# Optimization experiments

Hardware: AMD Instinct MI355X
Metric: run time of the kernel (lower is better)

The kernel has to match this reference:

```python
import jax, jax.numpy as jnp
import numpy as np

B, L, D, H = 8, 4096, 1024, 16
HD = D // H
HID = 4096  # int(D * 4.0)
KSZ = 25    # moving-average kernel size
EPS = 1e-6


def _layernorm(x, w, b):
    mu = jnp.mean(x, axis=-1, keepdims=True)
    var = jnp.mean((x - mu) ** 2, axis=-1, keepdims=True)
    return (x - mu) / jnp.sqrt(var + EPS) * w + b


def _lin(x, W, b):
    # eqx.nn.Linear stores weight as (out, in)
    return jnp.einsum('...i,oi->...o', x, W) + b


def setup_inputs() -> dict:
    key = jax.random.key(0)
    ks = jax.random.split(key, 8)
    s = 0.02
    return {
        'x': jax.random.normal(ks[0], (B, L, D), dtype=jnp.float32),
        'ln1_w': jnp.ones((D,), jnp.float32),
        'ln1_b': jnp.zeros((D,), jnp.float32),
        'Wq': jax.random.normal(ks[1], (D, D), jnp.float32) * s,
        'bq': jnp.zeros((D,), jnp.float32),
        'Wk': jax.random.normal(ks[2], (D, D), jnp.float32) * s,
        'bk': jnp.zeros((D,), jnp.float32),
        'Wv': jax.random.normal(ks[3], (D, D), jnp.float32) * s,
        'bv': jnp.zeros((D,), jnp.float32),
        'Wo': jax.random.normal(ks[4], (D, D), jnp.float32) * s,
        'bo': jnp.zeros((D,), jnp.float32),
        'ln2_w': jnp.ones((D,), jnp.float32),
        'ln2_b': jnp.zeros((D,), jnp.float32),
        'W1': jax.random.normal(ks[5], (HID, D), jnp.float32) * s,
        'b1': jnp.zeros((HID,), jnp.float32),
        'W2': jax.random.normal(ks[6], (D, HID), jnp.float32) * s,
        'b2': jnp.zeros((D,), jnp.float32),
    }


def reference(x, ln1_w, ln1_b, Wq, bq, Wk, bk, Wv, bv, Wo, bo,
              ln2_w, ln2_b, W1, b1, W2, b2):
    b, l, d = x.shape
    # --- AutoCorrelation attention on norm1(x) ---
    y = _layernorm(x, ln1_w, ln1_b)
    Q = _lin(y, Wq, bq).reshape(b, l, H, HD).transpose(0, 2, 1, 3)  # (B,H,L,hd)
    K = _lin(y, Wk, bk).reshape(b, l, H, HD).transpose(0, 2, 1, 3)
    V = _lin(y, Wv, bv).reshape(b, l, H, HD).transpose(0, 2, 1, 3)
    qf = jnp.fft.rfft(Q, axis=2)
    kf = jnp.fft.rfft(K, axis=2)
    corr_time = jnp.fft.irfft(qf * jnp.conjugate(kf), n=l, axis=2)  # (B,H,L,hd)
    corr = jnp.mean(corr_time, axis=-1)                             # (B,H,L)
    attn = jax.nn.softmax(corr, axis=-1)
    out = jnp.einsum('bhl,bhld->bhd', attn, V)                      # (B,H,hd)
    # faithful lossy reshape: transpose(0,2,1) -> (B,hd,H), flatten to (B,D)
    out = out.transpose(0, 2, 1).reshape(b, d)
    out = _lin(out, Wo, bo)
    y = jnp.broadcast_to(out[:, None, :], (b, l, d))  # repeat over L
    x = x + y
    # --- Series decomposition: depthwise moving average, subtract trend ---
    kern = jnp.ones((KSZ, 1, d), x.dtype) / KSZ
    xt = x.transpose(0, 2, 1)  # (B,D,L)
    trend = jax.lax.conv_general_dilated(
        xt, kern, window_strides=(1,), padding='SAME',
        dimension_numbers=('NCL', 'LIO', 'NCL'), feature_group_count=d)
    x = x - trend.transpose(0, 2, 1)
    # --- MLP (dropout p=0 -> identity) ---
    y = _layernorm(x, ln2_w, ln2_b)
    y = _lin(jax.nn.gelu(_lin(y, W1, b1)), W2, b2)
    return x + y
```

## Files before the change

### kernel.cpp

```cpp
#include <hip/hip_runtime.h>

#define DEV __device__ __forceinline__

typedef __attribute__((ext_vector_type(8))) short bf16x8;
typedef __attribute__((ext_vector_type(4))) float f32x4;
typedef unsigned short u16;
typedef __attribute__((address_space(1))) const void* gvp;
typedef __attribute__((address_space(3))) void* svp;

DEV u16 f2bf(float f){
  unsigned u = __float_as_uint(f);
  u = (u + 0x7FFFu + ((u >> 16) & 1u)) >> 16;
  return (u16)u;
}
DEV float bf2f(u16 v){ return __uint_as_float(((unsigned)v) << 16); }
DEV float2 cmul(float2 a, float2 b){ return make_float2(a.x*b.x - a.y*b.y, a.x*b.y + a.y*b.x); }
DEV int rev8(int i){
  return ((i & 7) << 9) | ((i & 0x38) << 3) | ((i & 0x1C0) >> 3) | ((i >> 9) & 7);
}

__global__ void k_prep(const float* __restrict__ Wq, const float* __restrict__ Wk,
                       const float* __restrict__ W1, const float* __restrict__ W2,
                       const float* __restrict__ bq, const float* __restrict__ bk,
                       u16* __restrict__ Wqkb, u16* __restrict__ W1b, u16* __restrict__ W2b,
                       float* __restrict__ bqk, float2* __restrict__ twg){
  const size_t i = (size_t)blockIdx.x * 256 + threadIdx.x;
  if (i < 1048576){
    Wqkb[i] = f2bf(Wq[i]);
  } else if (i < 2097152){
    Wqkb[i] = f2bf(Wk[i - 1048576]);
  } else if (i < 6291456){
    W1b[i - 2097152] = f2bf(W1[i - 2097152]);
  } else if (i < 10485760){
    W2b[i - 6291456] = f2bf(W2[i - 6291456]);
  } else if (i < 10487808){
    const int k = (int)(i - 10485760);
    float sn, cs;
    sincosf(-1.5339807878856412e-03f * (float)k, &sn, &cs);
    twg[k] = make_float2(cs, sn);
  } else if (i < 10488832){
    const int k = (int)(i - 10487808);
    bqk[k] = bq[k]; bqk[1024 + k] = bk[k];
  }
}

__global__ __launch_bounds__(256) void k_ln(const float* __restrict__ x, const float* __restrict__ w,
                                            const float* __restrict__ b, u16* __restrict__ y){
  const int row = blockIdx.x;
  const int tid = threadIdx.x;
  const float4 v = ((const float4*)(x + (size_t)row * 1024))[tid];
  float s1 = v.x + v.y + v.z + v.w;
  float s2 = v.x*v.x + v.y*v.y + v.z*v.z + v.w*v.w;
  #pragma unroll
  for (int o = 32; o > 0; o >>= 1){ s1 += __shfl_down(s1, o); s2 += __shfl_down(s2, o); }
  __shared__ float r1[4], r2[4];
  __shared__ float mu_s, rs_s;
  const int wv = tid >> 6;
  if ((tid & 63) == 0){ r1[wv] = s1; r2[wv] = s2; }
  __syncthreads();
  if (tid == 0){
    float t1 = r1[0]+r1[1]+r1[2]+r1[3], t2 = r2[0]+r2[1]+r2[2]+r2[3];
    float mu = t1 * (1.0f/1024.0f);
    float var = t2 * (1.0f/1024.0f) - mu*mu;
    mu_s = mu; rs_s = rsqrtf(var + 1e-6f);
  }
  __syncthreads();
  const float mu = mu_s, rs = rs_s;
  const float4 wv4 = ((const float4*)w)[tid];
  const float4 bv4 = ((const float4*)b)[tid];
  ushort4 o4;
  o4.x = f2bf((v.x-mu)*rs*wv4.x + bv4.x);
  o4.y = f2bf((v.y-mu)*rs*wv4.y + bv4.y);
  o4.z = f2bf((v.z-mu)*rs*wv4.z + bv4.z);
  o4.w = f2bf((v.w-mu)*rs*wv4.w + bv4.w);
  ((ushort4*)(y + (size_t)row*1024))[tid] = o4;
}

template<int MODE>
__launch_bounds__(512, 2)
__global__ void k_gemm5(const u16* __restrict__ A, const u16* __restrict__ Bw,
                        const float* __restrict__ bias, void* __restrict__ out, void* __restrict__ out2,
                        int M, int N, int K)
{
  __shared__ __align__(16) u16 SMEM[65536];
  u16 (*LA)[16384] = reinterpret_cast<u16(*)[16384]>(SMEM);
  u16 (*LB)[16384] = reinterpret_cast<u16(*)[16384]>(SMEM + 32768);
  const int tid = threadIdx.x;
  const int wave = tid >> 6, lane = tid & 63;
  const int l15 = lane & 15, l4 = lane >> 4;
  const int wrq = wave >> 2, wcq = wave & 3;
  (void)M;

  const int nwg = gridDim.x;
  const int q8 = nwg >> 3;
  const int wg = (blockIdx.x & 7) * q8 + (blockIdx.x >> 3);
  const int NBN = N >> 8;
  const int bm = wg / NBN, bn = wg % NBN;
  const int NT = K >> 6, NI = NT >> 1;

  const int sr8 = lane >> 3;
  const int sch8 = ((lane & 7) ^ (sr8 & 7)) * 8;
  const u16* gA = A  + ((size_t)(bm*256 + wave*16 + sr8)) * K + sch8;
  const u16* gB = Bw + ((size_t)(bn*256 + wave*16 + sr8)) * K + sch8;
  const size_t gH = (size_t)128 * K;
  const size_t gJ = (size_t)8 * K;
  const int lbase = wave * 1024;

  const unsigned swzb = (unsigned)((l4 ^ (l15 & 7)) * 16);
  const unsigned uA0  = (unsigned)(uintptr_t)&LA[0][0] + (unsigned)((wrq*64 + l15)*128) + swzb;
  const unsigned uB0  = (unsigned)(uintptr_t)&LB[0][0] + (unsigned)((wcq*32 + l15)*128) + swzb;
  const unsigned uA0x = uA0 ^ 64u, uB0x = uB0 ^ 64u;
  const unsigned uA1  = uA0 + 32768u, uA1x = uA0x + 32768u;
  const unsigned uB1  = uB0 + 32768u, uB1x = uB0x + 32768u;

  f32x4 acc[8][4];
  const f32x4 z4 = {0.f, 0.f, 0.f, 0.f};
  #pragma unroll
  for (int m = 0; m < 8; ++m)
    #pragma unroll
    for (int n = 0; n < 4; ++n) acc[m][n] = z4;

#define DSR(dst, base, OFF) asm volatile("ds_read_b128 %0, %1 offset:" #OFF : "=v"(dst) : "v"(base))

#define LDA_Q0(b0, b1) do{ \
  DSR(fa[0], b0, 0);    DSR(fa[1], b1, 0); \
  DSR(fa[2], b0, 2048); DSR(fa[3], b1, 2048); \
  DSR(fa[4], b0, 4096); DSR(fa[5], b1, 4096); \
  DSR(fa[6], b0, 6144); DSR(fa[7], b1, 6144); }while(0)
#define LDA_Q1(b0, b1) do{ \
  DSR(fa[0], b0, 16384); DSR(fa[1], b1, 16384); \
  DSR(fa[2], b0, 18432); DSR(fa[3], b1, 18432); \
  DSR(fa[4], b0, 20480); DSR(fa[5], b1, 20480); \
  DSR(fa[6], b0, 22528); DSR(fa[7], b1, 22528); }while(0)
#define LDB_Q0(dst, b0, b1) do{ \
  DSR(dst[0], b0, 0);    DSR(dst[1], b1, 0); \
  DSR(dst[2], b0, 2048); DSR(dst[3], b1, 2048); }while(0)
#define LDB_Q1(dst, b0, b1) do{ \
  DSR(dst[0], b0, 16384); DSR(dst[1], b1, 16384); \
  DSR(dst[2], b0, 18432); DSR(dst[3], b1, 18432); }while(0)

#define STG(LD, G, DB, HALF, TK) do{ \
    const int tk_ = (TK) < NT ? (TK) : NT - 1; \
    const u16* g_ = (G) + (size_t)tk_ * 64 + (size_t)(HALF) * gH; \
    u16* l_ = &LD[DB][lbase + (HALF) * 8192]; \
    __builtin_amdgcn_global_load_lds((gvp)g_,        (svp)l_,        16, 0, 0); \
    __builtin_amdgcn_global_load_lds((gvp)(g_ + gJ), (svp)(l_ + 512),16, 0, 0); \
  }while(0)

#define MFMA16(QA, QB, FB) do{ \
    __builtin_amdgcn_s_setprio(1); \
    _Pragma("unroll") for (int kk = 0; kk < 2; ++kk) \
    _Pragma("unroll") for (int mm = 0; mm < 4; ++mm) \
    _Pragma("unroll") for (int nn = 0; nn < 2; ++nn) \
      acc[(QA)*4+mm][(QB)*2+nn] = __builtin_amdgcn_mfma_f32_16x16x32_bf16( \
          fa[mm*2+kk], FB[nn*2+kk], acc[(QA)*4+mm][(QB)*2+nn], 0, 0, 0); \
    __builtin_amdgcn_s_setprio(0); \
  }while(0)

#define SBAR  __builtin_amdgcn_s_barrier()
#define SB0   __builtin_amdgcn_sched_barrier(0)
#define LGKM0 do{ asm volatile("s_waitcnt lgkmcnt(0)" ::: "memory"); SB0; }while(0)
#define LGKM8 asm volatile("s_waitcnt lgkmcnt(8)" ::: "memory")
#define VM4   asm volatile("s_waitcnt vmcnt(4)" ::: "memory")

  STG(LA, gA, 0, 0, 0); STG(LA, gA, 0, 1, 0);
  STG(LB, gB, 0, 0, 0); STG(LB, gB, 0, 1, 0);
  STG(LA, gA, 1, 0, 1);
  STG(LB, gB, 1, 1, 1);
  VM4; SBAR;

  for (int it = 0; it < NI; ++it){
    const int u = 2 * it;
    bf16x8 fa[8], fbA[4], fbB[4];
    LDB_Q0(fbA, uB0, uB0x);
    LDA_Q0(uA0, uA0x);
    STG(LA, gA, 1, 1, u+1); STG(LB, gB, 1, 0, u+1);
    LGKM8;
    SBAR; LGKM0; MFMA16(0, 0, fbA); SB0; SBAR;
    LDB_Q1(fbB, uB0, uB0x);
    SBAR; LGKM0; MFMA16(0, 1, fbB); SB0; SBAR;
    LDA_Q1(uA0, uA0x);
    STG(LA, gA, 0, 0, u+2);
    SBAR; LGKM0; MFMA16(1, 1, fbB); SB0; SBAR;
    STG(LB, gB, 0, 1, u+2);
    VM4; SBAR; SB0; MFMA16(1, 0, fbA); SB0; SBAR;
    LDB_Q0(fbA, uB1, uB1x);
    LDA_Q0(uA1, uA1x);
    STG(LA, gA, 0, 1, u+2); STG(LB, gB, 0, 0, u+2);
    LGKM8;
    SBAR; LGKM0; MFMA16(0, 0, fbA); SB0; SBAR;
    LDB_Q1(fbB, uB1, uB1x);
    SBAR; LGKM0; MFMA16(0, 1, fbB); SB0; SBAR;
    LDA_Q1(uA1, uA1x);
    STG(LA, gA, 1, 0, u+3);
    SBAR; LGKM0; MFMA16(1, 1, fbB); SB0; SBAR;
    STG(LB, gB, 1, 1, u+3);
    VM4; SBAR; SB0; MFMA16(1, 0, fbA); SB0; SBAR;
  }
#undef DSR
#undef LDA_Q0
#undef LDA_Q1
#undef LDB_Q0
#undef LDB_Q1
#undef STG
#undef MFMA16
#undef SBAR
#undef SB0
#undef LGKM0
#undef LGKM8
#undef VM4

  if (MODE == 3){
    asm volatile("s_waitcnt vmcnt(0)" ::: "memory");
    __syncthreads();
    u16* T = SMEM;
    const int bq = bm >> 4;
    const int l0 = (bm & 15) * 256;
    u16* dstb = (u16*)(bn < 4 ? out : out2) + ((size_t)bq*1024 + (bn & 3)*256)*4096 + l0;
    #pragma unroll
    for (int half = 0; half < 2; ++half){
      #pragma unroll
      for (int nn = 0; nn < 2; ++nn){
        const int n = half*2 + nn;
        const int colh = wcq*32 + nn*16 + l15;
        const float bv = bias[bn*256 + half*128 + colh];
        #pragma unroll
        for (int m = 0; m < 8; ++m){
          const int lrow = (m>>2)*128 + wrq*64 + (m&3)*16 + l4*4;
          ushort4 o4;
          o4.x = f2bf(acc[m][n][0] + bv);
          o4.y = f2bf(acc[m][n][1] + bv);
          o4.z = f2bf(acc[m][n][2] + bv);
          o4.w = f2bf(acc[m][n][3] + bv);
          *(ushort4*)&T[colh*264 + lrow] = o4;
        }
      }
      __syncthreads();
      {
        const int c = tid >> 2, lch = (tid & 3) * 64;
        u16* drow = dstb + (size_t)(half*128 + c) * 4096 + lch;
        const u16* srow = &T[c*264 + lch];
        #pragma unroll
        for (int i = 0; i < 8; ++i)
          *(bf16x8*)(drow + i*8) = *(const bf16x8*)(srow + i*8);
      }
      __syncthreads();
    }
  } else {
    #pragma unroll
    for (int m = 0; m < 8; ++m){
      const int gr0 = bm*256 + (m>>2)*128 + wrq*64 + (m&3)*16 + l4*4;
      #pragma unroll
      for (int n = 0; n < 4; ++n){
        const int gc = bn*256 + (n>>1)*128 + wcq*32 + (n&1)*16 + l15;
        const float bv = bias[gc];
        #pragma unroll
        for (int r2 = 0; r2 < 4; ++r2){
          const size_t off = (size_t)(gr0 + r2) * N + gc;
          float v = acc[m][n][r2] + bv;
          if (MODE == 1){
            const float a = 0.7978845608028654f * (v + 0.044715f * v * v * v);
            const float e = __expf(2.0f * a);
            const float th = (e - 1.0f) / (e + 1.0f);
            ((u16*)out)[off] = f2bf(0.5f * v * (1.0f + th));
          } else {
            float* op = (float*)out;
            op[off] += v;
          }
        }
      }
    }
  }
}

DEV void fft4096_dif8(float2* Z, const float2* tw, int tid){
  const float C = 0.70710678118654752f;
  #pragma unroll
  for (int s = 4; s >= 1; --s){
    const int q = 1 << (3*(s-1));
    const int step = 1 << (12 - 3*s);
    #pragma unroll
    for (int tt = tid; tt < 512; tt += 256){
      const int j = tt & (q-1);
      const int base = ((tt >> (3*(s-1))) << (3*s)) + j;
      float2 a0 = Z[base],       a1 = Z[base+q],   a2 = Z[base+2*q], a3 = Z[base+3*q];
      float2 a4 = Z[base+4*q],   a5 = Z[base+5*q], a6 = Z[base+6*q], a7 = Z[base+7*q];
      float2 e0 = {a0.x+a4.x, a0.y+a4.y}, o0 = {a0.x-a4.x, a0.y-a4.y};
      float2 e1 = {a2.x+a6.x, a2.y+a6.y}, o1 = {a2.x-a6.x, a2.y-a6.y};
      float2 e2 = {a1.x+a5.x, a1.y+a5.y}, o2 = {a1.x-a5.x, a1.y-a5.y};
      float2 e3 = {a3.x+a7.x, a3.y+a7.y}, o3 = {a3.x-a7.x, a3.y-a7.y};
      float2 E0 = {e0.x+e1.x, e0.y+e1.y}, E1 = {e0.x-e1.x, e0.y-e1.y};
      float2 E2 = {e2.x+e3.x, e2.y+e3.y}, E3 = {e2.x-e3.x, e2.y-e3.y};
      float2 u0 = {E0.x+E2.x, E0.y+E2.y};
      float2 u4 = {E0.x-E2.x, E0.y-E2.y};
      float2 njE3 = {E3.y, -E3.x};
      float2 u2 = {E1.x+njE3.x, E1.y+njE3.y};
      float2 u6 = {E1.x-njE3.x, E1.y-njE3.y};
      float2 W1o2 = {C*(o2.x+o2.y), C*(o2.y-o2.x)};
      float2 W3o2 = {C*(o2.y-o2.x), -C*(o2.x+o2.y)};
      float2 W1o3 = {C*(o3.x+o3.y), C*(o3.y-o3.x)};
      float2 W3o3 = {C*(o3.y-o3.x), -C*(o3.x+o3.y)};
      float2 njo1 = {o1.y, -o1.x};
      float2 u1 = {o0.x + W1o2.x + njo1.x + W3o3.x, o0.y + W1o2.y + njo1.y + W3o3.y};
      float2 u3 = {o0.x + W3o2.x - njo1.x + W1o3.x, o0.y + W3o2.y - njo1.y + W1o3.y};
      float2 u5 = {o0.x - W1o2.x + njo1.x - W3o3.x, o0.y - W1o2.y + njo1.y - W3o3.y};
      float2 u7 = {o0.x - W3o2.x - njo1.x - W1o3.x, o0.y - W3o2.y - njo1.y - W1o3.y};
      const float2 w1 = tw[j*step];
      const float2 w2 = tw[2*j*step];
      const float2 w4 = tw[4*j*step];
      const float2 w3 = cmul(w1, w2);
      const float2 w5 = cmul(w1, w4);
      const float2 w6 = cmul(w2, w4);
      const float2 w7 = cmul(w3, w4);
      Z[base]     = u0;
      Z[base+q]   = cmul(u1, w1);
      Z[base+2*q] = cmul(u2, w2);
      Z[base+3*q] = cmul(u3, w3);
      Z[base+4*q] = cmul(u4, w4);
      Z[base+5*q] = cmul(u5, w5);
      Z[base+6*q] = cmul(u6, w6);
      Z[base+7*q] = cmul(u7, w7);
    }
    __syncthreads();
  }
}

DEV void fft4096_dit8_inv(float2* Z, const float2* tw, int tid){
  const float C = 0.70710678118654752f;
  #pragma unroll
  for (int s = 1; s <= 4; ++s){
    const int q = 1 << (3*(s-1));
    const int step = 1 << (12 - 3*s);
    #pragma unroll
    for (int tt = tid; tt < 512; tt += 256){
      const int j = tt & (q-1);
      const int base = ((tt >> (3*(s-1))) << (3*s)) + j;
      float2 a0 = Z[base],       a1 = Z[base+q],   a2 = Z[base+2*q], a3 = Z[base+3*q];
      float2 a4 = Z[base+4*q],   a5 = Z[base+5*q], a6 = Z[base+6*q], a7 = Z[base+7*q];
      float2 w1 = tw[j*step];   w1.y = -w1.y;
      float2 w2 = tw[2*j*step]; w2.y = -w2.y;
      float2 w4 = tw[4*j*step]; w4.y = -w4.y;
      const float2 w3 = cmul(w1, w2);
      const float2 w5 = cmul(w1, w4);
      const float2 w6 = cmul(w2, w4);
      const float2 w7 = cmul(w3, w4);
      a1 = cmul(a1, w1); a2 = cmul(a2, w2); a3 = cmul(a3, w3);
      a4 = cmul(a4, w4); a5 = cmul(a5, w5); a6 = cmul(a6, w6); a7 = cmul(a7, w7);
      float2 e0 = {a0.x+a4.x, a0.y+a4.y}, o0 = {a0.x-a4.x, a0.y-a4.y};
      float2 e1 = {a2.x+a6.x, a2.y+a6.y}, o1 = {a2.x-a6.x, a2.y-a6.y};
      float2 e2 = {a1.x+a5.x, a1.y+a5.y}, o2 = {a1.x-a5.x, a1.y-a5.y};
      float2 e3 = {a3.x+a7.x, a3.y+a7.y}, o3 = {a3.x-a7.x, a3.y-a7.y};
      float2 E0 = {e0.x+e1.x, e0.y+e1.y}, E1 = {e0.x-e1.x, e0.y-e1.y};
      float2 E2 = {e2.x+e3.x, e2.y+e3.y}, E3 = {e2.x-e3.x, e2.y-e3.y};
      float2 pjE3 = {-E3.y, E3.x};
      float2 W1o2 = {C*(o2.x-o2.y), C*(o2.x+o2.y)};
      float2 W3o2 = {-C*(o2.x+o2.y), C*(o2.x-o2.y)};
      float2 W1o3 = {C*(o3.x-o3.y), C*(o3.x+o3.y)};
      float2 W3o3 = {-C*(o3.x+o3.y), C*(o3.x-o3.y)};
      float2 pjo1 = {-o1.y, o1.x};
      Z[base]     = make_float2(E0.x+E2.x, E0.y+E2.y);
      Z[base+q]   = make_float2(o0.x + W1o2.x + pjo1.x + W3o3.x, o0.y + W1o2.y + pjo1.y + W3o3.y);
      Z[base+2*q] = make_float2(E1.x+pjE3.x, E1.y+pjE3.y);
      Z[base+3*q] = make_float2(o0.x + W3o2.x - pjo1.x + W1o3.x, o0.y + W3o2.y - pjo1.y + W1o3.y);
      Z[base+4*q] = make_float2(E0.x-E2.x, E0.y-E2.y);
      Z[base+5*q] = make_float2(o0.x - W1o2.x + pjo1.x - W3o3.x, o0.y - W1o2.y + pjo1.y - W3o3.y);
      Z[base+6*q] = make_float2(E1.x-pjE3.x, E1.y-pjE3.y);
      Z[base+7*q] = make_float2(o0.x - W3o2.x - pjo1.x - W1o3.x, o0.y - W3o2.y - pjo1.y - W1o3.y);
    }
    __syncthreads();
  }
}

__global__ __launch_bounds__(256) void k_fftcorr(const u16* __restrict__ Qt, const u16* __restrict__ Kt,
                                                 const float2* __restrict__ twg, float* __restrict__ S){
  __shared__ float2 Z[4096];
  __shared__ float2 tw[2048];
  const int tid = threadIdx.x;
  const int bh = blockIdx.x, dg = blockIdx.y;
  for (int k = tid; k < 2048; k += 256) tw[k] = twg[k];
  float2 sa[16];
  #pragma unroll
  for (int j = 0; j < 16; ++j) sa[j] = make_float2(0.f, 0.f);
  __syncthreads();
  for (int dd = 0; dd < 8; ++dd){
    const int d = dg*8 + dd;
    const u16* q  = Qt + ((size_t)bh*64 + d) * 4096;
    const u16* kp = Kt + ((size_t)bh*64 + d) * 4096;
    for (int i = tid; i < 4096; i += 256)
      Z[i] = make_float2(bf2f(q[i]), bf2f(kp[i]));
    __syncthreads();
    fft4096_dif8(Z, tw, tid);
    #pragma unroll
    for (int j = 0; j < 16; ++j){
      const int p = j*256 + tid;
      const int f = rev8(p);
      const int p2 = rev8((4096 - f) & 4095);
      const float2 a = Z[p];
      const float2 c = Z[p2];
      const float qr = 0.5f * (a.x + c.x);
      const float qi = 0.5f * (a.y - c.y);
      const float kr = 0.5f * (a.y + c.y);
      const float ki = 0.5f * (c.x - a.x);
      sa[j].x += qr*kr + qi*ki;
      sa[j].y += qi*kr - qr*ki;
    }
    __syncthreads();
  }
  float2* Sg = (float2*)S + ((size_t)dg*128 + bh) * 4096;
  #pragma unroll
  for (int j = 0; j < 16; ++j)
    Sg[j*256 + tid] = sa[j];
}

__global__ __launch_bounds__(256) void k_isoftmax(const float* __restrict__ S, const float2* __restrict__ twg,
                                                  float* __restrict__ attn){
  __shared__ float2 Z[4096];
  __shared__ float2 tw[2048];
  __shared__ float red[4];
  __shared__ float bc;
  const int tid = threadIdx.x;
  const int bh = blockIdx.x;
  for (int k = tid; k < 2048; k += 256) tw[k] = twg[k];
  const float2* S2 = (const float2*)S;
  for (int i = tid; i < 4096; i += 256){
    float2 acc = make_float2(0.f, 0.f);
    #pragma unroll
    for (int g = 0; g < 8; ++g){
      const float2 v = S2[((size_t)g*128 + bh) * 4096 + i];
      acc.x += v.x; acc.y += v.y;
    }
    Z[i] = acc;
  }
  __syncthreads();
  fft4096_dit8_inv(Z, tw, tid);
  const float scale = 1.0f / (4096.0f * 64.0f);
  float cr[16];
  float lmax = -1e30f;
  #pragma unroll
  for (int j = 0; j < 16; ++j){
    const float c = Z[j*256 + tid].x * scale;
    cr[j] = c;
    lmax = fmaxf(lmax, c);
  }
  #pragma unroll
  for (int o = 32; o > 0; o >>= 1) lmax = fmaxf(lmax, __shfl_down(lmax, o));
  if ((tid & 63) == 0) red[tid >> 6] = lmax;
  __syncthreads();
  if (tid == 0) bc = fmaxf(fmaxf(red[0], red[1]), fmaxf(red[2], red[3]));
  __syncthreads();
  const float gmax = bc;
  float lsum = 0.f;
  #pragma unroll
  for (int j = 0; j < 16; ++j){ cr[j] = __expf(cr[j] - gmax); lsum += cr[j]; }
  #pragma unroll
  for (int o = 32; o > 0; o >>= 1) lsum += __shfl_down(lsum, o);
  if ((tid & 63) == 0) red[tid >> 6] = lsum;
  __syncthreads();
  if (tid == 0) bc = red[0] + red[1] + red[2] + red[3];
  __syncthreads();
  const float inv = 1.0f / bc;
  float* at = attn + (size_t)bh * 4096;
  #pragma unroll
  for (int j = 0; j < 16; ++j) at[j*256 + tid] = cr[j] * inv;
}

__global__ __launch_bounds__(256) void k_yw(const float* __restrict__ attn, const u16* __restrict__ Y,
                                            float* __restrict__ yw){
  __shared__ float at[128*20 + 4];
  const int b = blockIdx.x, lq = blockIdx.y;
  const int l0 = lq * 128;
  const int tid = threadIdx.x;
  for (int idx = tid; idx < 2048; idx += 256){
    const int h = idx >> 7, l = idx & 127;
    at[l*20 + h] = attn[((size_t)b*16 + h)*4096 + l0 + l];
  }
  __syncthreads();
  float acc[16][4];
  #pragma unroll
  for (int h = 0; h < 16; ++h)
    #pragma unroll
    for (int j = 0; j < 4; ++j) acc[h][j] = 0.f;
  const u16* yb = Y + ((size_t)b*4096 + l0)*1024 + tid*4;
  for (int l = 0; l < 128; ++l){
    const ushort4 yv4 = *(const ushort4*)(yb + (size_t)l*1024);
    const float y0 = bf2f(yv4.x), y1 = bf2f(yv4.y), y2 = bf2f(yv4.z), y3 = bf2f(yv4.w);
    #pragma unroll
    for (int hq = 0; hq < 4; ++hq){
      const float4 a4 = *(const float4*)&at[l*20 + hq*4];
      acc[hq*4+0][0] += a4.x*y0; acc[hq*4+0][1] += a4.x*y1; acc[hq*4+0][2] += a4.x*y2; acc[hq*4+0][3] += a4.x*y3;
      acc[hq*4+1][0] += a4.y*y0; acc[hq*4+1][1] += a4.y*y1; acc[hq*4+1][2] += a4.y*y2; acc[hq*4+1][3] += a4.y*y3;
      acc[hq*4+2][0] += a4.z*y0; acc[hq*4+2][1] += a4.z*y1; acc[hq*4+2][2] += a4.z*y2; acc[hq*4+2][3] += a4.z*y3;
      acc[hq*4+3][0] += a4.w*y0; acc[hq*4+3][1] += a4.w*y1; acc[hq*4+3][2] += a4.w*y2; acc[hq*4+3][3] += a4.w*y3;
    }
  }
  float* ywb = yw + (size_t)b*16*1024 + tid*4;
  #pragma unroll
  for (int h = 0; h < 16; ++h)
    #pragma unroll
    for (int j = 0; j < 4; ++j)
      atomicAdd(&ywb[(size_t)h*1024 + j], acc[h][j]);
}

__global__ __launch_bounds__(256) void k_vproj(const float* __restrict__ yw, const float* __restrict__ Wv,
                                               const float* __restrict__ bv, float* __restrict__ oav){
  __shared__ float yv[1024];
  const int b = blockIdx.x, h = blockIdx.y;
  const int tid = threadIdx.x;
  for (int i = tid; i < 1024; i += 256) yv[i] = yw[((size_t)b*16 + h)*1024 + i];
  __syncthreads();
  const int hd = tid >> 2, q = tid & 3;
  const float4* wr = (const float4*)(Wv + (size_t)(h*64 + hd)*1024 + q*256);
  float acc = 0.f;
  #pragma unroll 4
  for (int i = 0; i < 64; ++i){
    const float4 w4 = wr[i];
    acc += yv[q*256+4*i]*w4.x + yv[q*256+4*i+1]*w4.y + yv[q*256+4*i+2]*w4.z + yv[q*256+4*i+3]*w4.w;
  }
  acc += __shfl_xor(acc, 1);
  acc += __shfl_xor(acc, 2);
  if (q == 0) oav[(size_t)b*1024 + hd*16 + h] = acc + bv[h*64 + hd];
}

__global__ __launch_bounds__(256) void k_proj(const float* __restrict__ oav, const float* __restrict__ Wo,
                                              const float* __restrict__ bo, float* __restrict__ proj){
  const int b = blockIdx.x;
  const int o = blockIdx.y * 256 + threadIdx.x;
  __shared__ float xin[1024];
  for (int i = threadIdx.x; i < 1024; i += 256) xin[i] = oav[(size_t)b*1024 + i];
  __syncthreads();
  float acc = bo[o];
  const float4* wr = (const float4*)(Wo + (size_t)o * 1024);
  #pragma unroll 4
  for (int i = 0; i < 256; ++i){
    const float4 w4 = wr[i];
    acc += xin[4*i]*w4.x + xin[4*i+1]*w4.y + xin[4*i+2]*w4.z + xin[4*i+3]*w4.w;
  }
  proj[(size_t)b*1024 + o] = acc;
}

__global__ __launch_bounds__(256) void k_decomp(const float* __restrict__ x, const float* __restrict__ proj,
                                                float* __restrict__ out){
  const int b = blockIdx.x, dq = blockIdx.y, lc = blockIdx.z;
  const int d = dq*256 + threadIdx.x;
  const int l0 = lc * 128;
  const float pv = proj[(size_t)b*1024 + d];
  const float* xb = x + (size_t)b*4096*1024 + d;
  float* ob = out + (size_t)b*4096*1024 + d;
  if (lc == 0){
    float wsum = 0.f, cnt = 0.f;
    for (int j = 0; j <= 11; ++j){ wsum += xb[(size_t)j*1024]; cnt += 1.f; }
    for (int l = 0; l < 128; ++l){
      wsum += xb[(size_t)(l+12)*1024]; cnt += 1.f;
      const float xc = xb[(size_t)l*1024];
      ob[(size_t)l*1024] = xc + pv - (wsum + cnt*pv)*0.04f;
      if (l >= 12){ wsum -= xb[(size_t)(l-12)*1024]; cnt -= 1.f; }
    }
  } else if (lc == 31){
    float wsum = 0.f, cnt = 0.f;
    for (int j = l0-12; j <= l0+11; ++j){ wsum += xb[(size_t)j*1024]; cnt += 1.f; }
    for (int l = l0; l < 4096; ++l){
      if (l + 12 < 4096){ wsum += xb[(size_t)(l+12)*1024]; cnt += 1.f; }
      const float xc = xb[(size_t)l*1024];
      ob[(size_t)l*1024] = xc + pv - (wsum + cnt*pv)*0.04f;
      wsum -= xb[(size_t)(l-12)*1024]; cnt -= 1.f;
    }
  } else {
    float wsum = 0.f;
    #pragma unroll
    for (int j = -12; j <= 11; ++j) wsum += xb[(size_t)(l0+j)*1024];
    #pragma unroll 4
    for (int l = l0; l < l0 + 128; ++l){
      wsum += xb[(size_t)(l+12)*1024];
      const float xc = xb[(size_t)l*1024];
      ob[(size_t)l*1024] = xc - wsum*0.04f;
      wsum -= xb[(size_t)(l-12)*1024];
    }
  }
}

extern "C" void kernel_launch(void* const* d_in, const int* in_sizes, int n_in,
                              void* d_out, int out_size, void* d_ws, size_t ws_size,
                              hipStream_t stream){
  const float* x    = (const float*)d_in[0];
  const float* ln1w = (const float*)d_in[1];
  const float* ln1b = (const float*)d_in[2];
  const float* Wq   = (const float*)d_in[3];
  const float* bq   = (const float*)d_in[4];
  const float* Wk   = (const float*)d_in[5];
  const float* bk   = (const float*)d_in[6];
  const float* Wv   = (const float*)d_in[7];
  const float* bv   = (const float*)d_in[8];
  const float* Wo   = (const float*)d_in[9];
  const float* bo   = (const float*)d_in[10];
  const float* ln2w = (const float*)d_in[11];
  const float* ln2b = (const float*)d_in[12];
  const float* W1   = (const float*)d_in[13];
  const float* b1   = (const float*)d_in[14];
  const float* W2   = (const float*)d_in[15];
  const float* b2   = (const float*)d_in[16];
  float* out = (float*)d_out;

  char* ws = (char*)d_ws;
  float* S  = (float*)(ws + 0);
  u16* Qt   = (u16*)(ws + 134217728);
  u16* Kt   = (u16*)(ws + 201326592);
  u16* H1   = (u16*)(ws + 0);
  u16* Y    = (u16*)(ws + 268435456);
  float2* twg = (float2*)(ws + 339738624);
  float* attn = (float*)(ws + 339755008);
  float* yw   = (float*)(ws + 341852160);
  float* oav  = (float*)(ws + 342376448);
  float* proj = (float*)(ws + 342409216);
  float* bqk  = (float*)(ws + 342441984);
  u16* Wqkb   = (u16*)(ws + 342450176);
  u16* W1b    = (u16*)(ws + 346644480);
  u16* W2b    = (u16*)(ws + 355033088);

  k_prep<<<40972, 256, 0, stream>>>(Wq, Wk, W1, W2, bq, bk, Wqkb, W1b, W2b, bqk, twg);

  k_ln<<<32768, 256, 0, stream>>>(x, ln1w, ln1b, Y);

  k_gemm5<3><<<1024, 512, 0, stream>>>(Y, Wqkb, bqk, Qt, Kt, 32768, 2048, 1024);

  k_fftcorr<<<dim3(128, 8), 256, 0, stream>>>(Qt, Kt, twg, S);
  k_isoftmax<<<128, 256, 0, stream>>>(S, twg, attn);

  hipMemsetAsync(yw, 0, 524288, stream);
  k_yw<<<dim3(8, 32), 256, 0, stream>>>(attn, Y, yw);
  k_vproj<<<dim3(8, 16), 256, 0, stream>>>(yw, Wv, bv, oav);
  k_proj<<<dim3(8, 4), 256, 0, stream>>>(oav, Wo, bo, proj);

  k_decomp<<<dim3(8, 4, 32), 256, 0, stream>>>(x, proj, out);

  k_ln<<<32768, 256, 0, stream>>>(out, ln2w, ln2b, Y);

  k_gemm5<1><<<2048, 512, 0, stream>>>(Y, W1b, b1, H1, nullptr, 32768, 4096, 1024);
  k_gemm5<2><<<512, 512, 0, stream>>>(H1, W2b, b2, out, nullptr, 32768, 1024, 4096);
}
```

Baseline: 1.315 ms.

## Fuse series decomposition with second layernorm and read FFT twiddles from global

Replaces the separate moving-average decomposition kernel and the second layernorm kernel with one kernel. Each 512-thread block owns a 64-row strip and computes the decomposed row, its mean and variance, and the bf16 normalized output, so the decomposed activations are not reread from memory. The FFT kernels also stop staging twiddle factors in shared memory and read them directly from global memory through restrict pointers, which removes a shared-memory fill and one barrier. The cost is a launch of only 512 blocks with two barriers per row, which may limit parallelism, and twiddle reads that may now come from cache rather than LDS. The fused kernel also uses a one-pass variance formula.

```diff
diff --git a/kernel.cpp b/kernel.cpp
--- a/kernel.cpp
+++ b/kernel.cpp
@@ -273,7 +273,7 @@
   }
 }
 
-DEV void fft4096_dif8(float2* Z, const float2* tw, int tid){
+DEV void fft4096_dif8(float2* Z, const float2* __restrict__ tw, int tid){
   const float C = 0.70710678118654752f;
   #pragma unroll
   for (int s = 4; s >= 1; --s){
@@ -325,7 +325,7 @@
   }
 }
 
-DEV void fft4096_dit8_inv(float2* Z, const float2* tw, int tid){
+DEV void fft4096_dit8_inv(float2* Z, const float2* __restrict__ tw, int tid){
   const float C = 0.70710678118654752f;
   #pragma unroll
   for (int s = 1; s <= 4; ++s){
@@ -374,14 +374,11 @@
 __global__ __launch_bounds__(256) void k_fftcorr(const u16* __restrict__ Qt, const u16* __restrict__ Kt,
                                                  const float2* __restrict__ twg, float* __restrict__ S){
   __shared__ float2 Z[4096];
-  __shared__ float2 tw[2048];
   const int tid = threadIdx.x;
   const int bh = blockIdx.x, dg = blockIdx.y;
-  for (int k = tid; k < 2048; k += 256) tw[k] = twg[k];
   float2 sa[16];
   #pragma unroll
   for (int j = 0; j < 16; ++j) sa[j] = make_float2(0.f, 0.f);
-  __syncthreads();
   for (int dd = 0; dd < 8; ++dd){
     const int d = dg*8 + dd;
     const u16* q  = Qt + ((size_t)bh*64 + d) * 4096;
@@ -389,7 +386,7 @@
     for (int i = tid; i < 4096; i += 256)
       Z[i] = make_float2(bf2f(q[i]), bf2f(kp[i]));
     __syncthreads();
-    fft4096_dif8(Z, tw, tid);
+    fft4096_dif8(Z, twg, tid);
     #pragma unroll
     for (int j = 0; j < 16; ++j){
       const int p = j*256 + tid;
@@ -415,12 +412,10 @@
 __global__ __launch_bounds__(256) void k_isoftmax(const float* __restrict__ S, const float2* __restrict__ twg,
                                                   float* __restrict__ attn){
   __shared__ float2 Z[4096];
-  __shared__ float2 tw[2048];
   __shared__ float red[4];
   __shared__ float bc;
   const int tid = threadIdx.x;
   const int bh = blockIdx.x;
-  for (int k = tid; k < 2048; k += 256) tw[k] = twg[k];
   const float2* S2 = (const float2*)S;
   for (int i = tid; i < 4096; i += 256){
     float2 acc = make_float2(0.f, 0.f);
@@ -432,7 +427,7 @@
     Z[i] = acc;
   }
   __syncthreads();
-  fft4096_dit8_inv(Z, tw, tid);
+  fft4096_dit8_inv(Z, twg, tid);
   const float scale = 1.0f / (4096.0f * 64.0f);
   float cr[16];
   float lmax = -1e30f;
@@ -538,42 +533,67 @@
   proj[(size_t)b*1024 + o] = acc;
 }
 
-__global__ __launch_bounds__(256) void k_decomp(const float* __restrict__ x, const float* __restrict__ proj,
-                                                float* __restrict__ out){
-  const int b = blockIdx.x, dq = blockIdx.y, lc = blockIdx.z;
-  const int d = dq*256 + threadIdx.x;
-  const int l0 = lc * 128;
-  const float pv = proj[(size_t)b*1024 + d];
-  const float* xb = x + (size_t)b*4096*1024 + d;
-  float* ob = out + (size_t)b*4096*1024 + d;
-  if (lc == 0){
-    float wsum = 0.f, cnt = 0.f;
-    for (int j = 0; j <= 11; ++j){ wsum += xb[(size_t)j*1024]; cnt += 1.f; }
-    for (int l = 0; l < 128; ++l){
-      wsum += xb[(size_t)(l+12)*1024]; cnt += 1.f;
-      const float xc = xb[(size_t)l*1024];
-      ob[(size_t)l*1024] = xc + pv - (wsum + cnt*pv)*0.04f;
-      if (l >= 12){ wsum -= xb[(size_t)(l-12)*1024]; cnt -= 1.f; }
-    }
-  } else if (lc == 31){
-    float wsum = 0.f, cnt = 0.f;
-    for (int j = l0-12; j <= l0+11; ++j){ wsum += xb[(size_t)j*1024]; cnt += 1.f; }
-    for (int l = l0; l < 4096; ++l){
-      if (l + 12 < 4096){ wsum += xb[(size_t)(l+12)*1024]; cnt += 1.f; }
-      const float xc = xb[(size_t)l*1024];
-      ob[(size_t)l*1024] = xc + pv - (wsum + cnt*pv)*0.04f;
-      wsum -= xb[(size_t)(l-12)*1024]; cnt -= 1.f;
-    }
-  } else {
-    float wsum = 0.f;
-    #pragma unroll
-    for (int j = -12; j <= 11; ++j) wsum += xb[(size_t)(l0+j)*1024];
-    #pragma unroll 4
-    for (int l = l0; l < l0 + 128; ++l){
-      wsum += xb[(size_t)(l+12)*1024];
-      const float xc = xb[(size_t)l*1024];
-      ob[(size_t)l*1024] = xc - wsum*0.04f;
-      wsum -= xb[(size_t)(l-12)*1024];
+__global__ __launch_bounds__(512) void k_decln(const float* __restrict__ x, const float* __restrict__ proj,
+                                               const float* __restrict__ w, const float* __restrict__ bvec,
+                                               float* __restrict__ out, u16* __restrict__ y){
+  __shared__ float red1[8], red2[8];
+  __shared__ float mu_s, rs_s;
+  const int b = blockIdx.x, lc = blockIdx.y;
+  const int tid = threadIdx.x;
+  const int l0 = lc * 64;
+  const float* xb = x + (size_t)b*4096*1024;
+  float* ob = out + (size_t)b*4096*1024;
+  u16* yb = y + (size_t)b*4096*1024;
+  float pv[2], wv[2], bv[2], wsum[2];
+  #pragma unroll
+  for (int j = 0; j < 2; ++j){
+    const int d = tid + j*512;
+    pv[j] = proj[(size_t)b*1024 + d];
+    wv[j] = w[d]; bv[j] = bvec[d];
+    wsum[j] = 0.f;
+  }
+  float cnt = 0.f;
+  const int lo = (l0 - 12 < 0) ? 0 : l0 - 12;
+  for (int ll = lo; ll <= l0 + 11; ++ll){
+    #pragma unroll
+    for (int j = 0; j < 2; ++j) wsum[j] += xb[(size_t)ll*1024 + tid + j*512];
+    cnt += 1.f;
+  }
+  for (int l = l0; l < l0 + 64; ++l){
+    if (l + 12 < 4096){
+      #pragma unroll
+      for (int j = 0; j < 2; ++j) wsum[j] += xb[(size_t)(l+12)*1024 + tid + j*512];
+      cnt += 1.f;
+    }
+    float x2[2];
+    float s1 = 0.f, s2 = 0.f;
+    #pragma unroll
+    for (int j = 0; j < 2; ++j){
+      const float xc = xb[(size_t)l*1024 + tid + j*512];
+      x2[j] = xc + pv[j] - (wsum[j] + cnt*pv[j]) * 0.04f;
+      ob[(size_t)l*1024 + tid + j*512] = x2[j];
+      s1 += x2[j]; s2 += x2[j]*x2[j];
+    }
+    #pragma unroll
+    for (int o = 32; o > 0; o >>= 1){ s1 += __shfl_down(s1, o); s2 += __shfl_down(s2, o); }
+    if ((tid & 63) == 0){ red1[tid >> 6] = s1; red2[tid >> 6] = s2; }
+    __syncthreads();
+    if (tid == 0){
+      float t1 = 0.f, t2 = 0.f;
+      #pragma unroll
+      for (int k = 0; k < 8; ++k){ t1 += red1[k]; t2 += red2[k]; }
+      const float mu = t1 * (1.0f/1024.0f);
+      mu_s = mu; rs_s = rsqrtf(t2*(1.0f/1024.0f) - mu*mu + 1e-6f);
+    }
+    __syncthreads();
+    const float mu = mu_s, rs = rs_s;
+    #pragma unroll
+    for (int j = 0; j < 2; ++j)
+      yb[(size_t)l*1024 + tid + j*512] = f2bf((x2[j]-mu)*rs*wv[j] + bv[j]);
+    if (l >= 12){
+      #pragma unroll
+      for (int j = 0; j < 2; ++j) wsum[j] -= xb[(size_t)(l-12)*1024 + tid + j*512];
+      cnt -= 1.f;
     }
   }
 }
@@ -630,9 +650,7 @@
   k_vproj<<<dim3(8, 16), 256, 0, stream>>>(yw, Wv, bv, oav);
   k_proj<<<dim3(8, 4), 256, 0, stream>>>(oav, Wo, bo, proj);
 
-  k_decomp<<<dim3(8, 4, 32), 256, 0, stream>>>(x, proj, out);
-
-  k_ln<<<32768, 256, 0, stream>>>(out, ln2w, ln2b, Y);
+  k_decln<<<dim3(8, 64), 512, 0, stream>>>(x, proj, ln2w, ln2b, out, Y);
 
   k_gemm5<1><<<2048, 512, 0, stream>>>(Y, W1b, b1, H1, nullptr, 32768, 4096, 1024);
   k_gemm5<2><<<512, 512, 0, stream>>>(H1, W2b, b2, out, nullptr, 32768, 1024, 4096);
```

New measurement: 1.260 ms. -4.2%, faster.
